# Kernel tuning notes

Measured on AMD Instinct MI355X. Metric: run time of the kernel, lower is better.

The kernel has to match this reference:

```python
import jax, jax.numpy as jnp
import numpy as np

# CTBG circuit dims: units=[512,512,512], action_sz=6
UNIT1, UNIT2, UNIT3, ACTION = 512, 512, 512, 6
D_GPE_IN = UNIT1 * 3          # 1536  (striatum D1/D2/D3 blocks)
D_GPE_OUT = UNIT2 * 3         # 1536
D_GPI_IN = (UNIT1 + UNIT2) * 3  # 3072 (striatum + GPe/STN blocks)
D_GPI_OUT = UNIT2 * 3         # 1536
B = 16384


def setup_inputs() -> dict:
    key = jax.random.key(0)
    ks = jax.random.split(key, 12)
    x = jax.random.normal(ks[0], (B, D_GPE_IN), jnp.float32)
    # per-unit diagonal connectivity masks (unit_diags): [units, input_dim]
    gpe_mask = jax.random.bernoulli(ks[1], 0.5, (D_GPE_OUT, D_GPE_IN)).astype(jnp.float32)
    gpi_mask = jax.random.bernoulli(ks[2], 0.5, (D_GPI_OUT, D_GPI_IN)).astype(jnp.float32)
    # non-negative weights, uniform [0, 0.01) as in the TF initializer
    gpe_w = jax.random.uniform(ks[3], (D_GPE_IN, D_GPE_OUT), jnp.float32, 0.0, 0.01)
    gpe_b = jnp.zeros((D_GPE_OUT,), jnp.float32)
    gpi_w = jax.random.uniform(ks[4], (D_GPI_IN, D_GPI_OUT), jnp.float32, 0.0, 0.01)
    gpi_b = jnp.zeros((D_GPI_OUT,), jnp.float32)
    # Motor_cortex dense stack
    w1 = jax.random.normal(ks[5], (D_GPI_OUT, UNIT3), jnp.float32) / np.sqrt(D_GPI_OUT)
    b1 = jnp.zeros((UNIT3,), jnp.float32)
    w2 = jax.random.normal(ks[6], (UNIT3, UNIT3), jnp.float32) / np.sqrt(UNIT3)
    b2 = jnp.zeros((UNIT3,), jnp.float32)
    w3 = jax.random.normal(ks[7], (UNIT3, ACTION), jnp.float32) / np.sqrt(UNIT3)
    b3 = jnp.zeros((ACTION,), jnp.float32)
    return {"x": x, "gpe_mask": gpe_mask, "gpe_w": gpe_w, "gpe_b": gpe_b,
            "gpi_mask": gpi_mask, "gpi_w": gpi_w, "gpi_b": gpi_b,
            "w1": w1, "b1": b1, "w2": w2, "b2": b2, "w3": w3, "b3": b3}


def _masked_layer(x, mask, w, b):
    # TF original: p = transpose(matmul(diag(mask_u), x^T)) -> [B,U,I];
    #              f = diag_part(matmul(p, w)) + b
    # algebraically: f[b,u] = sum_i mask[u,i] * x[b,i] * w[i,u] + b[u]
    # which is a plain matmul against the element-wise masked weight.
    return x @ (w * mask.T) + b


def reference(x, gpe_mask, gpe_w, gpe_b, gpi_mask, gpi_w, gpi_b,
              w1, b1, w2, b2, w3, b3):
    gpe_out = _masked_layer(x, gpe_mask, gpe_w, gpe_b)          # [B, 1536]
    gpi_in = jnp.concatenate([x, gpe_out], axis=-1)              # [B, 3072]
    gpi_out = _masked_layer(gpi_in, gpi_mask, gpi_w, gpi_b)      # [B, 1536]
    h = jax.nn.relu(gpi_out @ w1 + b1)
    h = jax.nn.relu(h @ w2 + b2)
    return jax.nn.relu(h @ w3 + b3)                              # [B, 6]
```

## Files before the change

### kernel.cpp

```cpp
#include <hip/hip_runtime.h>
#include <stdint.h>


typedef __attribute__((ext_vector_type(8))) short short8;
typedef __attribute__((ext_vector_type(4))) float floatx4;

typedef const __attribute__((address_space(1))) void* gas1_cvp;
typedef __attribute__((address_space(3))) void* gas3_vp;

__device__ __forceinline__ void load_lds16(const void* g, void* s) {
    __builtin_amdgcn_global_load_lds((gas1_cvp)g, (gas3_vp)s, 16, 0, 0);
}

__device__ __forceinline__ unsigned short f2bf(float f) {
    unsigned int u = __float_as_uint(f);
    u = u + 0x7fffu + ((u >> 16) & 1u);
    return (unsigned short)(u >> 16);
}
__device__ __forceinline__ float bf2f(unsigned short h) {
    return __uint_as_float(((unsigned int)h) << 16);
}
__device__ __forceinline__ short8 cvt8(float4 a, float4 b) {
    short8 r;
    r[0] = (short)f2bf(a.x); r[1] = (short)f2bf(a.y);
    r[2] = (short)f2bf(a.z); r[3] = (short)f2bf(a.w);
    r[4] = (short)f2bf(b.x); r[5] = (short)f2bf(b.y);
    r[6] = (short)f2bf(b.z); r[7] = (short)f2bf(b.w);
    return r;
}

__device__ __forceinline__ void dev_prep_t(
        float (*tile)[65],
        const float* __restrict__ w, const float* __restrict__ mask,
        unsigned short* __restrict__ out,
        int ldw, int ldm, int ldo, int bx, int by) {
    int n0 = bx * 64;
    int k0 = by * 64;
    int t = threadIdx.x;
    int c4 = (t & 15) * 4;
    int r  = t >> 4;

    #pragma unroll
    for (int p = 0; p < 4; ++p) {
        int kk = r + p * 16;
        float4 v = *(const float4*)(w + (size_t)(k0 + kk) * ldw + n0 + c4);
        tile[c4 + 0][kk] = v.x;
        tile[c4 + 1][kk] = v.y;
        tile[c4 + 2][kk] = v.z;
        tile[c4 + 3][kk] = v.w;
    }
    __syncthreads();
    #pragma unroll
    for (int p = 0; p < 4; ++p) {
        int nn = r + p * 16;
        float mx = 1.f, my = 1.f, mz = 1.f, mw = 1.f;
        if (mask) {
            float4 m = *(const float4*)(mask + (size_t)(n0 + nn) * ldm + k0 + c4);
            mx = m.x; my = m.y; mz = m.z; mw = m.w;
        }
        ushort4 o;
        o.x = f2bf(tile[nn][c4 + 0] * mx);
        o.y = f2bf(tile[nn][c4 + 1] * my);
        o.z = f2bf(tile[nn][c4 + 2] * mz);
        o.w = f2bf(tile[nn][c4 + 3] * mw);
        *(ushort4*)(out + (size_t)(n0 + nn) * ldo + k0 + c4) = o;
    }
}

__device__ __forceinline__ void dev_prep_nt(
        float (*tile)[65],
        const float* __restrict__ w, const float* __restrict__ mask,
        unsigned short* __restrict__ out,
        int ldw, int ldm, int ldo, int bx, int by) {
    int j0 = bx * 64;
    int i0 = by * 64;
    int t = threadIdx.x;
    int c4 = (t & 15) * 4;
    int r  = t >> 4;

    #pragma unroll
    for (int p = 0; p < 4; ++p) {
        int jj = r + p * 16;
        float4 m = *(const float4*)(mask + (size_t)(j0 + jj) * ldm + i0 + c4);
        tile[c4 + 0][jj] = m.x;
        tile[c4 + 1][jj] = m.y;
        tile[c4 + 2][jj] = m.z;
        tile[c4 + 3][jj] = m.w;
    }
    __syncthreads();
    #pragma unroll
    for (int p = 0; p < 4; ++p) {
        int ii = r + p * 16;
        float4 v = *(const float4*)(w + (size_t)(i0 + ii) * ldw + j0 + c4);
        ushort4 o;
        o.x = f2bf(v.x * tile[ii][c4 + 0]);
        o.y = f2bf(v.y * tile[ii][c4 + 1]);
        o.z = f2bf(v.z * tile[ii][c4 + 2]);
        o.w = f2bf(v.w * tile[ii][c4 + 3]);
        *(ushort4*)(out + (size_t)(i0 + ii) * ldo + j0 + c4) = o;
    }
}

__global__ __launch_bounds__(256) void prep_all_kernel(
        const float* __restrict__ gpe_w, const float* __restrict__ gpe_mask,
        const float* __restrict__ gpi_w, const float* __restrict__ gpi_mask,
        const float* __restrict__ w1, const float* __restrict__ w2,
        unsigned short* __restrict__ wi_topnt, unsigned short* __restrict__ wibot_ui,
        unsigned short* __restrict__ we_nt, unsigned short* __restrict__ w1t,
        unsigned short* __restrict__ w2t, float* __restrict__ zero_base) {
    __shared__ float tile[64][65];
    int b = blockIdx.x;
    if (b < 576) {
        dev_prep_nt(tile, gpi_w, gpi_mask, wi_topnt, 1536, 3072, 1536,
                    b % 24, b / 24);
    } else if (b < 1152) {
        int lb = b - 576;
        dev_prep_nt(tile, gpi_w + (size_t)1536 * 1536, gpi_mask + 1536, wibot_ui,
                    1536, 3072, 1536, lb % 24, lb / 24);
    } else if (b < 1728) {
        int lb = b - 1152;
        dev_prep_nt(tile, gpe_w, gpe_mask, we_nt, 1536, 1536, 1536,
                    lb % 24, lb / 24);
    } else if (b < 1920) {
        int lb = b - 1728;
        dev_prep_t(tile, w1, nullptr, w1t, 512, 0, 1536, lb % 8, lb / 8);
    } else if (b < 1984) {
        int lb = b - 1920;
        dev_prep_t(tile, w2, nullptr, w2t, 512, 0, 512, lb % 8, lb / 8);
    } else {
        float4 z = {0.f, 0.f, 0.f, 0.f};
        float* p = zero_base + (size_t)(b - 1984) * 4096 + threadIdx.x * 16;
        #pragma unroll
        for (int i = 0; i < 4; ++i) *(float4*)(p + i * 4) = z;
    }
}

template <bool F32A>
__device__ __forceinline__ void dev_combine_splitk(
        unsigned short* As, unsigned short* Bs,
        const void* __restrict__ Aop,
        const unsigned short* __restrict__ B,
        float* __restrict__ C,
        int kbase, int ntl, int bx, int by) {
    const int m0 = by * 64;
    const int n0 = bx * 128;
    const int t    = threadIdx.x;
    const int lane = t & 63;
    const int w    = t >> 6;
    const int wm   = w >> 1;
    const int wn   = w & 1;
    const int lm   = lane & 15;
    const int lq   = lane >> 4;

    const int srow = lane >> 2;
    const int scol = (lane & 3) * 8;

    size_t aidx[2];
    int rbA[2], awr[2];
    #pragma unroll
    for (int i = 0; i < 2; ++i) {
        aidx[i] = (size_t)(m0 + w * 16 + srow) * 1536 + i * 32 + scol + kbase;
        rbA[i]  = i * 2048 + w * 512;
        awr[i]  = i * 2048 + (w * 16 + srow) * 32 + scol;
    }
    size_t bidx[4];
    int rbB[4];
    #pragma unroll
    for (int i = 0; i < 4; ++i) {
        int rows = w * 32 + (i >> 1) * 16;
        bidx[i] = (size_t)(n0 + rows + srow) * 1536 + (i & 1) * 32 + scol + kbase;
        rbB[i]  = (i & 1) * 4096 + rows * 32;
    }

    int aro[2][2], bro[2][4];
    #pragma unroll
    for (int ks = 0; ks < 2; ++ks) {
        #pragma unroll
        for (int mi = 0; mi < 2; ++mi)
            aro[ks][mi] = ks * 2048 + (wm * 32 + mi * 16 + lm) * 32 + lq * 8;
        #pragma unroll
        for (int ni = 0; ni < 4; ++ni)
            bro[ks][ni] = ks * 4096 + (wn * 64 + ni * 16 + lm) * 32 + lq * 8;
    }

    const float* Af = (const float*)Aop;
    const unsigned short* Ab = (const unsigned short*)Aop;

    floatx4 acc[2][4] = {};
    float4 ra[2][2];

    #pragma unroll
    for (int i = 0; i < 4; ++i) load_lds16(B + bidx[i], Bs + rbB[i]);
    if (F32A) {
        #pragma unroll
        for (int i = 0; i < 2; ++i) {
            ra[i][0] = *(const float4*)(Af + aidx[i]);
            ra[i][1] = *(const float4*)(Af + aidx[i] + 4);
        }
        #pragma unroll
        for (int i = 0; i < 2; ++i)
            *(short8*)(As + awr[i]) = cvt8(ra[i][0], ra[i][1]);
    } else {
        #pragma unroll
        for (int i = 0; i < 2; ++i) load_lds16(Ab + aidx[i], As + rbA[i]);
    }
    __syncthreads();

    int buf = 0;
    for (int tt = 0; tt < ntl; ++tt) {
        const int kn = (tt + 1) << 6;
        const int more = tt + 1 < ntl;
        if (more) {
            const int nbA = (buf ^ 1) * 4096;
            const int nbB = (buf ^ 1) * 8192;
            #pragma unroll
            for (int i = 0; i < 4; ++i)
                load_lds16(B + bidx[i] + kn, Bs + nbB + rbB[i]);
            if (F32A) {
                #pragma unroll
                for (int i = 0; i < 2; ++i) {
                    ra[i][0] = *(const float4*)(Af + aidx[i] + kn);
                    ra[i][1] = *(const float4*)(Af + aidx[i] + kn + 4);
                }
            } else {
                #pragma unroll
                for (int i = 0; i < 2; ++i)
                    load_lds16(Ab + aidx[i] + kn, As + nbA + rbA[i]);
            }
        }
        const int cA = buf * 4096, cB = buf * 8192;
        #pragma unroll
        for (int ks = 0; ks < 2; ++ks) {
            short8 af[2], bf8[4];
            #pragma unroll
            for (int mi = 0; mi < 2; ++mi)
                af[mi] = *(const short8*)(As + cA + aro[ks][mi]);
            #pragma unroll
            for (int ni = 0; ni < 4; ++ni)
                bf8[ni] = *(const short8*)(Bs + cB + bro[ks][ni]);
            #pragma unroll
            for (int mi = 0; mi < 2; ++mi)
                #pragma unroll
                for (int ni = 0; ni < 4; ++ni)
                    acc[mi][ni] = __builtin_amdgcn_mfma_f32_16x16x32_bf16(
                        af[mi], bf8[ni], acc[mi][ni], 0, 0, 0);
        }
        if (more) {
            if (F32A) {
                const int nbA = (buf ^ 1) * 4096;
                #pragma unroll
                for (int i = 0; i < 2; ++i)
                    *(short8*)(As + nbA + awr[i]) = cvt8(ra[i][0], ra[i][1]);
            }
            __syncthreads();
        }
        buf ^= 1;
    }

    #pragma unroll
    for (int mi = 0; mi < 2; ++mi) {
        int rbase = m0 + wm * 32 + mi * 16 + lq * 4;
        #pragma unroll
        for (int ni = 0; ni < 4; ++ni) {
            int cc = n0 + wn * 64 + ni * 16 + lm;
            #pragma unroll
            for (int r = 0; r < 4; ++r)
                unsafeAtomicAdd(&C[(size_t)(rbase + r) * 1536 + cc],
                                acc[mi][ni][r]);
        }
    }
}

__global__ __launch_bounds__(256) void combineA_kernel(
        const unsigned short* __restrict__ w1t,
        const unsigned short* __restrict__ wibot_ui,
        float* __restrict__ t1f) {
    __shared__ unsigned short As[2 * 4096];
    __shared__ unsigned short Bs[2 * 8192];
    int b = blockIdx.x;
    int s = b / 96;
    int r = b % 96;
    dev_combine_splitk<false>(As, Bs, w1t, wibot_ui, t1f,
                              s * 512, 8, r % 12, r / 12);
}

__global__ __launch_bounds__(256) void combineB_kernel(
        const unsigned short* __restrict__ w1t,
        const unsigned short* __restrict__ wi_topnt,
        const float* __restrict__ t1f,
        const unsigned short* __restrict__ we_nt,
        float* __restrict__ w1cf) {
    __shared__ unsigned short As[2 * 4096];
    __shared__ unsigned short Bs[2 * 8192];
    int b = blockIdx.x;
    int c = b / 96;
    int r = b % 96;
    int kbase = (c % 3) * 512;
    if (c < 3) {
        dev_combine_splitk<false>(As, Bs, w1t, wi_topnt, w1cf,
                                  kbase, 8, r % 12, r / 12);
    } else {
        dev_combine_splitk<true>(As, Bs, t1f, we_nt, w1cf,
                                 kbase, 8, r % 12, r / 12);
    }
}

__global__ __launch_bounds__(256) void finalize_kernel(
        const float* __restrict__ w1cf, unsigned short* __restrict__ w1ct,
        const unsigned short* __restrict__ w1t, const float* __restrict__ t1f,
        const float* __restrict__ gpi_b, const float* __restrict__ gpe_b,
        const float* __restrict__ b1, float* __restrict__ b1c) {
    int b = blockIdx.x;
    if (b < 384) {
        size_t base = (size_t)b * 2048 + threadIdx.x * 8;
        float4 v0 = *(const float4*)(w1cf + base);
        float4 v1 = *(const float4*)(w1cf + base + 4);
        ushort4 o0, o1;
        o0.x = f2bf(v0.x); o0.y = f2bf(v0.y); o0.z = f2bf(v0.z); o0.w = f2bf(v0.w);
        o1.x = f2bf(v1.x); o1.y = f2bf(v1.y); o1.z = f2bf(v1.z); o1.w = f2bf(v1.w);
        *(ushort4*)(w1ct + base) = o0;
        *(ushort4*)(w1ct + base + 4) = o1;
    } else {
        int n = (b - 384) * 4 + (threadIdx.x >> 6);
        int lane = threadIdx.x & 63;
        const unsigned short* r1 = w1t + (size_t)n * 1536;
        const float* r2 = t1f + (size_t)n * 1536;
        float s = 0.f;
        for (int i = lane; i < 1536; i += 64)
            s += gpi_b[i] * bf2f(r1[i]) + gpe_b[i] * r2[i];
        #pragma unroll
        for (int off = 32; off; off >>= 1) s += __shfl_down(s, off, 64);
        if (lane == 0) b1c[n] = b1[n] + s;
    }
}

__global__ __launch_bounds__(256) void gemm_a32_kernel(
        const float* __restrict__ A,
        const unsigned short* __restrict__ Bt,
        const float* __restrict__ bias,
        unsigned short* __restrict__ C,
        int K, int lda, int ldc) {
    __shared__ unsigned short As[2 * 2048];
    __shared__ unsigned short Bs[2 * 4096];

    const int bid = blockIdx.x;
    const int idx = bid >> 3;
    const int m0 = ((bid & 7) * 32 + (idx >> 2)) * 64;
    const int n0 = (idx & 3) * 128;

    const int t    = threadIdx.x;
    const int lane = t & 63;
    const int w    = t >> 6;
    const int wm   = w >> 1;
    const int wn   = w & 1;
    const int lm   = lane & 15;
    const int lq   = lane >> 4;

    const int arow = t >> 2;
    const int acol = (t & 3) * 8;
    const float* ag = A + (size_t)(m0 + arow) * lda + acol;
    const int awr = arow * 32 + acol;

    const unsigned short* bg[2];
    int rbB[2];
    #pragma unroll
    for (int j = 0; j < 2; ++j) {
        int c = w * 2 + j;
        bg[j]  = Bt + (size_t)(n0 + c * 16 + (lane >> 2)) * K + (lane & 3) * 8;
        rbB[j] = c * 512;
    }

    int aro[2], bro[4];
    #pragma unroll
    for (int mi = 0; mi < 2; ++mi)
        aro[mi] = (wm * 32 + mi * 16 + lm) * 32 + lq * 8;
    #pragma unroll
    for (int ni = 0; ni < 4; ++ni)
        bro[ni] = (wn * 64 + ni * 16 + lm) * 32 + lq * 8;

    floatx4 acc[2][4] = {};
    float4 ra0, ra1;

    load_lds16(bg[0], Bs + rbB[0]);
    load_lds16(bg[1], Bs + rbB[1]);
    ra0 = *(const float4*)(ag);
    ra1 = *(const float4*)(ag + 4);
    *(short8*)(As + awr) = cvt8(ra0, ra1);
    __syncthreads();

    const int nt = K >> 5;
    int buf = 0;
    for (int tt = 0; tt < nt; ++tt) {
        const int kn = (tt + 1) << 5;
        const bool more = kn < K;
        if (more) {
            const int nbB = (buf ^ 1) * 4096;
            load_lds16(bg[0] + kn, Bs + nbB + rbB[0]);
            load_lds16(bg[1] + kn, Bs + nbB + rbB[1]);
            ra0 = *(const float4*)(ag + kn);
            ra1 = *(const float4*)(ag + kn + 4);
        }
        const int cA = buf * 2048, cB = buf * 4096;
        short8 af[2], bf8[4];
        #pragma unroll
        for (int mi = 0; mi < 2; ++mi)
            af[mi] = *(const short8*)(As + cA + aro[mi]);
        #pragma unroll
        for (int ni = 0; ni < 4; ++ni)
            bf8[ni] = *(const short8*)(Bs + cB + bro[ni]);
        #pragma unroll
        for (int mi = 0; mi < 2; ++mi)
            #pragma unroll
            for (int ni = 0; ni < 4; ++ni)
                acc[mi][ni] = __builtin_amdgcn_mfma_f32_16x16x32_bf16(
                    af[mi], bf8[ni], acc[mi][ni], 0, 0, 0);
        if (more) {
            *(short8*)(As + (buf ^ 1) * 2048 + awr) = cvt8(ra0, ra1);
            __syncthreads();
        }
        buf ^= 1;
    }

    float bv[4];
    #pragma unroll
    for (int ni = 0; ni < 4; ++ni) bv[ni] = bias[n0 + wn * 64 + ni * 16 + lm];

    #pragma unroll
    for (int mi = 0; mi < 2; ++mi) {
        int rbase = m0 + wm * 32 + mi * 16 + lq * 4;
        #pragma unroll
        for (int ni = 0; ni < 4; ++ni) {
            int cc = n0 + wn * 64 + ni * 16 + lm;
            #pragma unroll
            for (int r = 0; r < 4; ++r) {
                float v = fmaxf(acc[mi][ni][r] + bv[ni], 0.f);
                C[(size_t)(rbase + r) * ldc + cc] = f2bf(v);
            }
        }
    }
}

__global__ __launch_bounds__(256) void gemm_bt_kernel(
        const unsigned short* __restrict__ A,
        const unsigned short* __restrict__ Bt,
        const float* __restrict__ bias,
        unsigned short* __restrict__ C,
        int K, int lda, int ldc) {
    __shared__ unsigned short As[2 * 2048];
    __shared__ unsigned short Bs[2 * 4096];

    const int bid = blockIdx.x;
    const int idx = bid >> 3;
    const int m0 = ((bid & 7) * 32 + (idx >> 2)) * 64;
    const int n0 = (idx & 3) * 128;

    const int t    = threadIdx.x;
    const int lane = t & 63;
    const int w    = t >> 6;
    const int wm   = w >> 1;
    const int wn   = w & 1;
    const int lm   = lane & 15;
    const int lq   = lane >> 4;

    const unsigned short* ag =
        A + (size_t)(m0 + w * 16 + (lane >> 2)) * lda + (lane & 3) * 8;
    const int rbA = w * 512;

    const unsigned short* bg[2];
    int rbB[2];
    #pragma unroll
    for (int j = 0; j < 2; ++j) {
        int c = w * 2 + j;
        bg[j]  = Bt + (size_t)(n0 + c * 16 + (lane >> 2)) * K + (lane & 3) * 8;
        rbB[j] = c * 512;
    }

    int aro[2], bro[4];
    #pragma unroll
    for (int mi = 0; mi < 2; ++mi)
        aro[mi] = (wm * 32 + mi * 16 + lm) * 32 + lq * 8;
    #pragma unroll
    for (int ni = 0; ni < 4; ++ni)
        bro[ni] = (wn * 64 + ni * 16 + lm) * 32 + lq * 8;

    floatx4 acc[2][4] = {};

    load_lds16(ag, As + rbA);
    load_lds16(bg[0], Bs + rbB[0]);
    load_lds16(bg[1], Bs + rbB[1]);
    __syncthreads();

    const int nt = K >> 5;
    int buf = 0;
    for (int tt = 0; tt < nt; ++tt) {
        const int kn = (tt + 1) << 5;
        const bool more = kn < K;
        if (more) {
            const int nbA = (buf ^ 1) * 2048;
            const int nbB = (buf ^ 1) * 4096;
            load_lds16(ag + kn, As + nbA + rbA);
            load_lds16(bg[0] + kn, Bs + nbB + rbB[0]);
            load_lds16(bg[1] + kn, Bs + nbB + rbB[1]);
        }
        const int cA = buf * 2048, cB = buf * 4096;
        short8 af[2], bf8[4];
        #pragma unroll
        for (int mi = 0; mi < 2; ++mi)
            af[mi] = *(const short8*)(As + cA + aro[mi]);
        #pragma unroll
        for (int ni = 0; ni < 4; ++ni)
            bf8[ni] = *(const short8*)(Bs + cB + bro[ni]);
        #pragma unroll
        for (int mi = 0; mi < 2; ++mi)
            #pragma unroll
            for (int ni = 0; ni < 4; ++ni)
                acc[mi][ni] = __builtin_amdgcn_mfma_f32_16x16x32_bf16(
                    af[mi], bf8[ni], acc[mi][ni], 0, 0, 0);
        if (more) __syncthreads();
        buf ^= 1;
    }

    float bv[4];
    #pragma unroll
    for (int ni = 0; ni < 4; ++ni) bv[ni] = bias[n0 + wn * 64 + ni * 16 + lm];

    #pragma unroll
    for (int mi = 0; mi < 2; ++mi) {
        int rbase = m0 + wm * 32 + mi * 16 + lq * 4;
        #pragma unroll
        for (int ni = 0; ni < 4; ++ni) {
            int cc = n0 + wn * 64 + ni * 16 + lm;
            #pragma unroll
            for (int r = 0; r < 4; ++r) {
                float v = fmaxf(acc[mi][ni][r] + bv[ni], 0.f);
                C[(size_t)(rbase + r) * ldc + cc] = f2bf(v);
            }
        }
    }
}

__global__ void head_kernel(const unsigned short* __restrict__ h,
                            const float* __restrict__ w3,
                            const float* __restrict__ b3,
                            float* __restrict__ out) {
    int row = blockIdx.x * 4 + (threadIdx.x >> 6);
    int lane = threadIdx.x & 63;
    const unsigned short* hp = h + (size_t)row * 512 + lane * 8;
    ushort4 ha = *(const ushort4*)(hp);
    ushort4 hb = *(const ushort4*)(hp + 4);
    float hv[8] = {bf2f(ha.x), bf2f(ha.y), bf2f(ha.z), bf2f(ha.w),
                   bf2f(hb.x), bf2f(hb.y), bf2f(hb.z), bf2f(hb.w)};
    const float* wp = w3 + lane * 48;
    float s[6] = {0.f, 0.f, 0.f, 0.f, 0.f, 0.f};
    #pragma unroll
    for (int j = 0; j < 8; ++j)
        #pragma unroll
        for (int a = 0; a < 6; ++a)
            s[a] += hv[j] * wp[j * 6 + a];
    #pragma unroll
    for (int a = 0; a < 6; ++a)
        #pragma unroll
        for (int off = 32; off; off >>= 1)
            s[a] += __shfl_down(s[a], off, 64);
    if (lane == 0) {
        #pragma unroll
        for (int a = 0; a < 6; ++a)
            out[(size_t)row * 6 + a] = fmaxf(s[a] + b3[a], 0.f);
    }
}

extern "C" void kernel_launch(void* const* d_in, const int* in_sizes, int n_in,
                              void* d_out, int out_size, void* d_ws, size_t ws_size,
                              hipStream_t stream) {
    const float* x        = (const float*)d_in[0];
    const float* gpe_mask = (const float*)d_in[1];
    const float* gpe_w    = (const float*)d_in[2];
    const float* gpe_b    = (const float*)d_in[3];
    const float* gpi_mask = (const float*)d_in[4];
    const float* gpi_w    = (const float*)d_in[5];
    const float* gpi_b    = (const float*)d_in[6];
    const float* w1       = (const float*)d_in[7];
    const float* b1       = (const float*)d_in[8];
    const float* w2       = (const float*)d_in[9];
    const float* b2       = (const float*)d_in[10];
    const float* w3       = (const float*)d_in[11];
    const float* b3       = (const float*)d_in[12];
    float* out = (float*)d_out;

    char* ws = (char*)d_ws;
    unsigned short* h1        = (unsigned short*)(ws);
    unsigned short* h2        = (unsigned short*)(ws + 16777216);
    float*          t1f       = (float*)(ws + 16777216);
    float*          w1cf      = (float*)(ws + 19922944);
    unsigned short* wi_topnt  = (unsigned short*)(ws + 33554432);
    unsigned short* wibot_ui  = (unsigned short*)(ws + 38273024);
    unsigned short* we_nt     = (unsigned short*)(ws + 42991616);
    unsigned short* w1t       = (unsigned short*)(ws + 47710208);
    unsigned short* w2t       = (unsigned short*)(ws + 49283072);
    unsigned short* w1ct      = (unsigned short*)(ws + 49807360);
    float*          b1c       = (float*)(ws + 51380224);

    prep_all_kernel<<<dim3(2368), dim3(256), 0, stream>>>(
        gpe_w, gpe_mask, gpi_w, gpi_mask, w1, w2,
        wi_topnt, wibot_ui, we_nt, w1t, w2t, t1f);

    combineA_kernel<<<dim3(288), dim3(256), 0, stream>>>(w1t, wibot_ui, t1f);

    combineB_kernel<<<dim3(576), dim3(256), 0, stream>>>(
        w1t, wi_topnt, t1f, we_nt, w1cf);

    finalize_kernel<<<dim3(512), dim3(256), 0, stream>>>(
        w1cf, w1ct, w1t, t1f, gpi_b, gpe_b, b1, b1c);

    gemm_a32_kernel<<<dim3(1024), dim3(256), 0, stream>>>(
        x, w1ct, b1c, h1, 1536, 1536, 512);
    gemm_bt_kernel<<<dim3(1024), dim3(256), 0, stream>>>(
        h1, w2t, b2, h2, 512, 512, 512);
    head_kernel<<<dim3(16384 / 4), dim3(256), 0, stream>>>(h2, w3, b3, out);
}
```

Before: 350.5 us.

## Fuse first GEMM, second GEMM and action head into one LDS-resident kernel

Replaces the three separate kernels (fp32-A GEMM, bf16 GEMM, head) with one kernel in which each 512-thread block owns 64 rows and all 512 output columns. The first-layer activations stay in LDS and feed the second GEMM directly, and the 6-wide head is reduced in registers and LDS. This removes the h1/h2 round trips to global memory and two launches. In exchange only 256 blocks run, one per CU, with about 137KB of LDS and 16 accumulator tiles per wave, so occupancy and latency hiding drop.

```diff
diff --git a/kernel.cpp b/kernel.cpp
--- a/kernel.cpp
+++ b/kernel.cpp
@@ -27,6 +27,11 @@
     r[4] = (short)f2bf(b.x); r[5] = (short)f2bf(b.y);
     r[6] = (short)f2bf(b.z); r[7] = (short)f2bf(b.w);
     return r;
+}
+__device__ __forceinline__ ushort4 cvt4(float4 a) {
+    ushort4 o;
+    o.x = f2bf(a.x); o.y = f2bf(a.y); o.z = f2bf(a.z); o.w = f2bf(a.w);
+    return o;
 }
 
 __device__ __forceinline__ void dev_prep_t(
@@ -334,20 +339,23 @@
     }
 }
 
-__global__ __launch_bounds__(256) void gemm_a32_kernel(
-        const float* __restrict__ A,
-        const unsigned short* __restrict__ Bt,
-        const float* __restrict__ bias,
-        unsigned short* __restrict__ C,
-        int K, int lda, int ldc) {
-    __shared__ unsigned short As[2 * 2048];
-    __shared__ unsigned short Bs[2 * 4096];
-
-    const int bid = blockIdx.x;
-    const int idx = bid >> 3;
-    const int m0 = ((bid & 7) * 32 + (idx >> 2)) * 64;
-    const int n0 = (idx & 3) * 128;
-
+__global__ __launch_bounds__(512, 1) void fused_mlp_kernel(
+        const float* __restrict__ x,
+        const unsigned short* __restrict__ w1ct,
+        const float* __restrict__ b1c,
+        const unsigned short* __restrict__ w2t,
+        const float* __restrict__ b2,
+        const float* __restrict__ w3,
+        const float* __restrict__ b3,
+        float* __restrict__ out) {
+    __shared__ __align__(16) unsigned char lds_raw[140288];
+    unsigned short* Bs  = (unsigned short*)lds_raw;
+    unsigned short* As  = (unsigned short*)(lds_raw + 65536);
+    unsigned short* H1  = (unsigned short*)(lds_raw + 73728);
+    float* w3s = (float*)lds_raw;
+    float* red = (float*)(lds_raw + 16384);
+
+    const int m0   = blockIdx.x * 64;
     const int t    = threadIdx.x;
     const int lane = t & 63;
     const int w    = t >> 6;
@@ -356,216 +364,147 @@
     const int lm   = lane & 15;
     const int lq   = lane >> 4;
 
-    const int arow = t >> 2;
-    const int acol = (t & 3) * 8;
-    const float* ag = A + (size_t)(m0 + arow) * lda + acol;
-    const int awr = arow * 32 + acol;
-
-    const unsigned short* bg[2];
-    int rbB[2];
-    #pragma unroll
-    for (int j = 0; j < 2; ++j) {
-        int c = w * 2 + j;
-        bg[j]  = Bt + (size_t)(n0 + c * 16 + (lane >> 2)) * K + (lane & 3) * 8;
-        rbB[j] = c * 512;
-    }
-
-    int aro[2], bro[4];
-    #pragma unroll
-    for (int mi = 0; mi < 2; ++mi)
-        aro[mi] = (wm * 32 + mi * 16 + lm) * 32 + lq * 8;
-    #pragma unroll
-    for (int ni = 0; ni < 4; ++ni)
-        bro[ni] = (wn * 64 + ni * 16 + lm) * 32 + lq * 8;
-
-    floatx4 acc[2][4] = {};
-    float4 ra0, ra1;
-
-    load_lds16(bg[0], Bs + rbB[0]);
-    load_lds16(bg[1], Bs + rbB[1]);
-    ra0 = *(const float4*)(ag);
-    ra1 = *(const float4*)(ag + 4);
-    *(short8*)(As + awr) = cvt8(ra0, ra1);
-    __syncthreads();
-
-    const int nt = K >> 5;
-    int buf = 0;
-    for (int tt = 0; tt < nt; ++tt) {
+    const unsigned short* bg1[4];
+    const unsigned short* bg2[4];
+    int rbB[4];
+    #pragma unroll
+    for (int j = 0; j < 4; ++j) {
+        int row = w * 64 + j * 16 + (lane >> 2);
+        bg1[j] = w1ct + (size_t)row * 1536 + (lane & 3) * 8;
+        bg2[j] = w2t  + (size_t)row * 512  + (lane & 3) * 8;
+        rbB[j] = w * 2048 + j * 512;
+    }
+    const float* ag = x + (size_t)(m0 + (t >> 3)) * 1536 + (t & 7) * 4;
+    const int awr = (t >> 3) * 32 + (t & 7) * 4;
+
+    const int aro = (wm * 16 + lm) * 32 + lq * 8;
+    int bro[16];
+    #pragma unroll
+    for (int ni = 0; ni < 16; ++ni)
+        bro[ni] = (wn * 256 + ni * 16 + lm) * 32 + lq * 8;
+
+    floatx4 acc[16];
+    #pragma unroll
+    for (int ni = 0; ni < 16; ++ni) acc[ni] = (floatx4){0.f, 0.f, 0.f, 0.f};
+
+    float4 ra = *(const float4*)ag;
+    #pragma unroll
+    for (int j = 0; j < 4; ++j) load_lds16(bg1[j], Bs + rbB[j]);
+    *(ushort4*)(As + awr) = cvt4(ra);
+    __syncthreads();
+
+    for (int tt = 0; tt < 48; ++tt) {
         const int kn = (tt + 1) << 5;
-        const bool more = kn < K;
+        const bool more = tt + 1 < 48;
+        const int nbB = ((tt + 1) & 1) * 16384;
+        const int nbA = ((tt + 1) & 1) * 2048;
         if (more) {
-            const int nbB = (buf ^ 1) * 4096;
-            load_lds16(bg[0] + kn, Bs + nbB + rbB[0]);
-            load_lds16(bg[1] + kn, Bs + nbB + rbB[1]);
-            ra0 = *(const float4*)(ag + kn);
-            ra1 = *(const float4*)(ag + kn + 4);
-        }
-        const int cA = buf * 2048, cB = buf * 4096;
-        short8 af[2], bf8[4];
-        #pragma unroll
-        for (int mi = 0; mi < 2; ++mi)
-            af[mi] = *(const short8*)(As + cA + aro[mi]);
-        #pragma unroll
-        for (int ni = 0; ni < 4; ++ni)
-            bf8[ni] = *(const short8*)(Bs + cB + bro[ni]);
-        #pragma unroll
-        for (int mi = 0; mi < 2; ++mi)
-            #pragma unroll
-            for (int ni = 0; ni < 4; ++ni)
-                acc[mi][ni] = __builtin_amdgcn_mfma_f32_16x16x32_bf16(
-                    af[mi], bf8[ni], acc[mi][ni], 0, 0, 0);
+            #pragma unroll
+            for (int j = 0; j < 4; ++j)
+                load_lds16(bg1[j] + kn, Bs + nbB + rbB[j]);
+            ra = *(const float4*)(ag + kn);
+        }
+        const int cB = (tt & 1) * 16384;
+        const int cA = (tt & 1) * 2048;
+        short8 af = *(const short8*)(As + cA + aro);
+        #pragma unroll
+        for (int ni = 0; ni < 16; ++ni) {
+            short8 bf = *(const short8*)(Bs + cB + bro[ni]);
+            acc[ni] = __builtin_amdgcn_mfma_f32_16x16x32_bf16(
+                af, bf, acc[ni], 0, 0, 0);
+        }
         if (more) {
-            *(short8*)(As + (buf ^ 1) * 2048 + awr) = cvt8(ra0, ra1);
+            *(ushort4*)(As + nbA + awr) = cvt4(ra);
             __syncthreads();
         }
-        buf ^= 1;
-    }
-
-    float bv[4];
-    #pragma unroll
-    for (int ni = 0; ni < 4; ++ni) bv[ni] = bias[n0 + wn * 64 + ni * 16 + lm];
-
-    #pragma unroll
-    for (int mi = 0; mi < 2; ++mi) {
-        int rbase = m0 + wm * 32 + mi * 16 + lq * 4;
-        #pragma unroll
-        for (int ni = 0; ni < 4; ++ni) {
-            int cc = n0 + wn * 64 + ni * 16 + lm;
-            #pragma unroll
-            for (int r = 0; r < 4; ++r) {
-                float v = fmaxf(acc[mi][ni][r] + bv[ni], 0.f);
-                C[(size_t)(rbase + r) * ldc + cc] = f2bf(v);
-            }
-        }
-    }
-}
-
-__global__ __launch_bounds__(256) void gemm_bt_kernel(
-        const unsigned short* __restrict__ A,
-        const unsigned short* __restrict__ Bt,
-        const float* __restrict__ bias,
-        unsigned short* __restrict__ C,
-        int K, int lda, int ldc) {
-    __shared__ unsigned short As[2 * 2048];
-    __shared__ unsigned short Bs[2 * 4096];
-
-    const int bid = blockIdx.x;
-    const int idx = bid >> 3;
-    const int m0 = ((bid & 7) * 32 + (idx >> 2)) * 64;
-    const int n0 = (idx & 3) * 128;
-
-    const int t    = threadIdx.x;
-    const int lane = t & 63;
-    const int w    = t >> 6;
-    const int wm   = w >> 1;
-    const int wn   = w & 1;
-    const int lm   = lane & 15;
-    const int lq   = lane >> 4;
-
-    const unsigned short* ag =
-        A + (size_t)(m0 + w * 16 + (lane >> 2)) * lda + (lane & 3) * 8;
-    const int rbA = w * 512;
-
-    const unsigned short* bg[2];
-    int rbB[2];
-    #pragma unroll
-    for (int j = 0; j < 2; ++j) {
-        int c = w * 2 + j;
-        bg[j]  = Bt + (size_t)(n0 + c * 16 + (lane >> 2)) * K + (lane & 3) * 8;
-        rbB[j] = c * 512;
-    }
-
-    int aro[2], bro[4];
-    #pragma unroll
-    for (int mi = 0; mi < 2; ++mi)
-        aro[mi] = (wm * 32 + mi * 16 + lm) * 32 + lq * 8;
-    #pragma unroll
-    for (int ni = 0; ni < 4; ++ni)
-        bro[ni] = (wn * 64 + ni * 16 + lm) * 32 + lq * 8;
-
-    floatx4 acc[2][4] = {};
-
-    load_lds16(ag, As + rbA);
-    load_lds16(bg[0], Bs + rbB[0]);
-    load_lds16(bg[1], Bs + rbB[1]);
-    __syncthreads();
-
-    const int nt = K >> 5;
-    int buf = 0;
-    for (int tt = 0; tt < nt; ++tt) {
+    }
+
+    #pragma unroll
+    for (int ni = 0; ni < 16; ++ni) {
+        const int col = wn * 256 + ni * 16 + lm;
+        const float bv = b1c[col];
+        #pragma unroll
+        for (int r = 0; r < 4; ++r) {
+            const int row = wm * 16 + lq * 4 + r;
+            H1[row * 520 + col] = f2bf(fmaxf(acc[ni][r] + bv, 0.f));
+        }
+    }
+    #pragma unroll
+    for (int j = 0; j < 4; ++j) load_lds16(bg2[j], Bs + rbB[j]);
+    __syncthreads();
+
+    #pragma unroll
+    for (int ni = 0; ni < 16; ++ni) acc[ni] = (floatx4){0.f, 0.f, 0.f, 0.f};
+
+    const int h1row = (wm * 16 + lm) * 520;
+    for (int tt = 0; tt < 16; ++tt) {
         const int kn = (tt + 1) << 5;
-        const bool more = kn < K;
+        const bool more = tt + 1 < 16;
+        const int nbB = ((tt + 1) & 1) * 16384;
         if (more) {
-            const int nbA = (buf ^ 1) * 2048;
-            const int nbB = (buf ^ 1) * 4096;
-            load_lds16(ag + kn, As + nbA + rbA);
-            load_lds16(bg[0] + kn, Bs + nbB + rbB[0]);
-            load_lds16(bg[1] + kn, Bs + nbB + rbB[1]);
-        }
-        const int cA = buf * 2048, cB = buf * 4096;
-        short8 af[2], bf8[4];
-        #pragma unroll
-        for (int mi = 0; mi < 2; ++mi)
-            af[mi] = *(const short8*)(As + cA + aro[mi]);
-        #pragma unroll
-        for (int ni = 0; ni < 4; ++ni)
-            bf8[ni] = *(const short8*)(Bs + cB + bro[ni]);
-        #pragma unroll
-        for (int mi = 0; mi < 2; ++mi)
-            #pragma unroll
-            for (int ni = 0; ni < 4; ++ni)
-                acc[mi][ni] = __builtin_amdgcn_mfma_f32_16x16x32_bf16(
-                    af[mi], bf8[ni], acc[mi][ni], 0, 0, 0);
+            #pragma unroll
+            for (int j = 0; j < 4; ++j)
+                load_lds16(bg2[j] + kn, Bs + nbB + rbB[j]);
+        }
+        const int cB = (tt & 1) * 16384;
+        short8 af = *(const short8*)(H1 + h1row + tt * 32 + lq * 8);
+        #pragma unroll
+        for (int ni = 0; ni < 16; ++ni) {
+            short8 bf = *(const short8*)(Bs + cB + bro[ni]);
+            acc[ni] = __builtin_amdgcn_mfma_f32_16x16x32_bf16(
+                af, bf, acc[ni], 0, 0, 0);
+        }
         if (more) __syncthreads();
-        buf ^= 1;
-    }
-
-    float bv[4];
-    #pragma unroll
-    for (int ni = 0; ni < 4; ++ni) bv[ni] = bias[n0 + wn * 64 + ni * 16 + lm];
-
-    #pragma unroll
-    for (int mi = 0; mi < 2; ++mi) {
-        int rbase = m0 + wm * 32 + mi * 16 + lq * 4;
-        #pragma unroll
-        for (int ni = 0; ni < 4; ++ni) {
-            int cc = n0 + wn * 64 + ni * 16 + lm;
-            #pragma unroll
-            for (int r = 0; r < 4; ++r) {
-                float v = fmaxf(acc[mi][ni][r] + bv[ni], 0.f);
-                C[(size_t)(rbase + r) * ldc + cc] = f2bf(v);
-            }
-        }
-    }
-}
-
-__global__ void head_kernel(const unsigned short* __restrict__ h,
-                            const float* __restrict__ w3,
-                            const float* __restrict__ b3,
-                            float* __restrict__ out) {
-    int row = blockIdx.x * 4 + (threadIdx.x >> 6);
-    int lane = threadIdx.x & 63;
-    const unsigned short* hp = h + (size_t)row * 512 + lane * 8;
-    ushort4 ha = *(const ushort4*)(hp);
-    ushort4 hb = *(const ushort4*)(hp + 4);
-    float hv[8] = {bf2f(ha.x), bf2f(ha.y), bf2f(ha.z), bf2f(ha.w),
-                   bf2f(hb.x), bf2f(hb.y), bf2f(hb.z), bf2f(hb.w)};
-    const float* wp = w3 + lane * 48;
-    float s[6] = {0.f, 0.f, 0.f, 0.f, 0.f, 0.f};
-    #pragma unroll
-    for (int j = 0; j < 8; ++j)
-        #pragma unroll
-        for (int a = 0; a < 6; ++a)
-            s[a] += hv[j] * wp[j * 6 + a];
-    #pragma unroll
-    for (int a = 0; a < 6; ++a)
-        #pragma unroll
-        for (int off = 32; off; off >>= 1)
-            s[a] += __shfl_down(s[a], off, 64);
-    if (lane == 0) {
-        #pragma unroll
-        for (int a = 0; a < 6; ++a)
-            out[(size_t)row * 6 + a] = fmaxf(s[a] + b3[a], 0.f);
+    }
+
+    {
+        const float* src = w3 + t * 6;
+        #pragma unroll
+        for (int a = 0; a < 6; ++a) w3s[t * 6 + a] = src[a];
+    }
+    __syncthreads();
+
+    float part[4][6] = {};
+    #pragma unroll
+    for (int ni = 0; ni < 16; ++ni) {
+        const int col = wn * 256 + ni * 16 + lm;
+        const float b2v = b2[col];
+        float wv[6];
+        #pragma unroll
+        for (int a = 0; a < 6; ++a) wv[a] = w3s[col * 6 + a];
+        #pragma unroll
+        for (int r = 0; r < 4; ++r) {
+            const float h = fmaxf(acc[ni][r] + b2v, 0.f);
+            #pragma unroll
+            for (int a = 0; a < 6; ++a) part[r][a] += h * wv[a];
+        }
+    }
+    #pragma unroll
+    for (int off = 1; off <= 8; off <<= 1)
+        #pragma unroll
+        for (int r = 0; r < 4; ++r)
+            #pragma unroll
+            for (int a = 0; a < 6; ++a)
+                part[r][a] += __shfl_xor(part[r][a], off, 64);
+
+    if (wn == 0 && lm == 0) {
+        #pragma unroll
+        for (int r = 0; r < 4; ++r) {
+            const int row = wm * 16 + lq * 4 + r;
+            #pragma unroll
+            for (int a = 0; a < 6; ++a) red[row * 6 + a] = part[r][a];
+        }
+    }
+    __syncthreads();
+    if (wn == 1 && lm == 0) {
+        #pragma unroll
+        for (int r = 0; r < 4; ++r) {
+            const int row = wm * 16 + lq * 4 + r;
+            #pragma unroll
+            for (int a = 0; a < 6; ++a)
+                out[(size_t)(m0 + row) * 6 + a] =
+                    fmaxf(red[row * 6 + a] + part[r][a] + b3[a], 0.f);
+        }
     }
 }
 
@@ -588,8 +527,6 @@
     float* out = (float*)d_out;
 
     char* ws = (char*)d_ws;
-    unsigned short* h1        = (unsigned short*)(ws);
-    unsigned short* h2        = (unsigned short*)(ws + 16777216);
     float*          t1f       = (float*)(ws + 16777216);
     float*          w1cf      = (float*)(ws + 19922944);
     unsigned short* wi_topnt  = (unsigned short*)(ws + 33554432);
@@ -612,9 +549,6 @@
     finalize_kernel<<<dim3(512), dim3(256), 0, stream>>>(
         w1cf, w1ct, w1t, t1f, gpi_b, gpe_b, b1, b1c);
 
-    gemm_a32_kernel<<<dim3(1024), dim3(256), 0, stream>>>(
-        x, w1ct, b1c, h1, 1536, 1536, 512);
-    gemm_bt_kernel<<<dim3(1024), dim3(256), 0, stream>>>(
-        h1, w2t, b2, h2, 512, 512, 512);
-    head_kernel<<<dim3(16384 / 4), dim3(256), 0, stream>>>(h2, w3, b3, out);
-}
+    fused_mlp_kernel<<<dim3(256), dim3(512), 0, stream>>>(
+        x, w1ct, b1c, w2t, b2, w3, b3, out);
+}
```

Measured after the change: 315.2 us. -10.1%, faster.
